# Kernel tuning notes

Hardware: AMD Instinct MI355X
Metric: run time of the kernel (lower is better)

## Reference

```python
import jax, jax.numpy as jnp
import numpy as np

NUM_NODES = 100000
NUM_EDGES = 1600000
INPUT_DIM = 128
HIDDEN_DIM = 64
OUTPUT_DIM = 2
DROPOUT_P = 0.5


def setup_inputs() -> dict:
    key = jax.random.key(0)
    ks = jax.random.split(key, 6)
    x = jax.random.normal(ks[0], (NUM_NODES, INPUT_DIM), dtype=jnp.float32)
    edge_index = jax.random.randint(ks[1], (2, NUM_EDGES), 0, NUM_NODES, dtype=jnp.int64)
    W_conv = jax.random.normal(ks[2], (INPUT_DIM, HIDDEN_DIM), dtype=jnp.float32) * (1.0 / np.sqrt(INPUT_DIM))
    b_conv = jax.random.normal(ks[3], (HIDDEN_DIM,), dtype=jnp.float32) * 0.02
    W_lin = jax.random.normal(ks[4], (HIDDEN_DIM, OUTPUT_DIM), dtype=jnp.float32) * (1.0 / np.sqrt(HIDDEN_DIM))
    b_lin = jax.random.normal(ks[5], (OUTPUT_DIM,), dtype=jnp.float32) * 0.02
    return {"x": x, "edge_index": edge_index, "W_conv": W_conv, "b_conv": b_conv,
            "W_lin": W_lin, "b_lin": b_lin}


def _gcn_conv(x, edge_index, W, b):
    n = x.shape[0]
    # linear transform first (PyG GCNConv)
    h = x @ W  # [N, hidden]
    # add self-loops
    loop = jnp.arange(n, dtype=edge_index.dtype)
    row = jnp.concatenate([edge_index[0], loop])  # source
    col = jnp.concatenate([edge_index[1], loop])  # target
    # symmetric normalization deg^{-1/2} (degree counted on targets, incl. self-loops)
    deg = jax.ops.segment_sum(jnp.ones_like(col, dtype=h.dtype), col, num_segments=n)
    dinv = jnp.where(deg > 0, jax.lax.rsqrt(deg), 0.0)
    norm = dinv[row] * dinv[col]  # [E+N]
    # gather -> scale -> scatter-add
    msgs = h[row] * norm[:, None]  # [E+N, hidden]
    out = jax.ops.segment_sum(msgs, col, num_segments=n)
    return out + b


def reference(x, edge_index, W_conv, b_conv, W_lin, b_lin):
    h = _gcn_conv(x, edge_index, W_conv, b_conv)
    h = jax.nn.relu(h)
    # dropout p=0.5, training mode, deterministic key for reproducibility
    keep = jax.random.bernoulli(jax.random.key(42), 1.0 - DROPOUT_P, h.shape)
    h = jnp.where(keep, h / (1.0 - DROPOUT_P), 0.0)
    return h @ W_lin + b_lin
```

## Files before the change

kernel.cpp:

```cpp
#include <hip/hip_runtime.h>
#include <hip/hip_bf16.h>

#define N_NODES 100000
#define N_EDGES 1600000
#define IN_DIM 128
#define HID 64
#define NB 391
#define EPB 4096
#define BUCKET_BLOCKS ((N_EDGES + EPB - 1) / EPB)
#define MAXPB 8192
#define WTE (HID * 136)

typedef __attribute__((ext_vector_type(8))) short bf16x8;
typedef __attribute__((ext_vector_type(4))) float f32x4;

__device__ __forceinline__ unsigned rotl32(unsigned x, unsigned r) {
    return (x << r) | (x >> (32u - r));
}

__device__ __forceinline__ void threefry2x32_k42(unsigned x0, unsigned x1,
                                                 unsigned& o0, unsigned& o1) {
    const unsigned ks0 = 0u;
    const unsigned ks1 = 42u;
    const unsigned ks2 = 0u ^ 42u ^ 0x1BD11BDAu;
    x0 += ks0; x1 += ks1;
    x0 += x1; x1 = rotl32(x1, 13); x1 ^= x0;
    x0 += x1; x1 = rotl32(x1, 15); x1 ^= x0;
    x0 += x1; x1 = rotl32(x1, 26); x1 ^= x0;
    x0 += x1; x1 = rotl32(x1, 6);  x1 ^= x0;
    x0 += ks1; x1 += ks2 + 1u;
    x0 += x1; x1 = rotl32(x1, 17); x1 ^= x0;
    x0 += x1; x1 = rotl32(x1, 29); x1 ^= x0;
    x0 += x1; x1 = rotl32(x1, 16); x1 ^= x0;
    x0 += x1; x1 = rotl32(x1, 24); x1 ^= x0;
    x0 += ks2; x1 += ks0 + 2u;
    x0 += x1; x1 = rotl32(x1, 13); x1 ^= x0;
    x0 += x1; x1 = rotl32(x1, 15); x1 ^= x0;
    x0 += x1; x1 = rotl32(x1, 26); x1 ^= x0;
    x0 += x1; x1 = rotl32(x1, 6);  x1 ^= x0;
    x0 += ks0; x1 += ks1 + 3u;
    x0 += x1; x1 = rotl32(x1, 17); x1 ^= x0;
    x0 += x1; x1 = rotl32(x1, 29); x1 ^= x0;
    x0 += x1; x1 = rotl32(x1, 16); x1 ^= x0;
    x0 += x1; x1 = rotl32(x1, 24); x1 ^= x0;
    x0 += ks1; x1 += ks2 + 4u;
    x0 += x1; x1 = rotl32(x1, 13); x1 ^= x0;
    x0 += x1; x1 = rotl32(x1, 15); x1 ^= x0;
    x0 += x1; x1 = rotl32(x1, 26); x1 ^= x0;
    x0 += x1; x1 = rotl32(x1, 6);  x1 ^= x0;
    x0 += ks2; x1 += ks0 + 5u;
    o0 = x0; o1 = x1;
}

__device__ __forceinline__ float bf2f(unsigned short u) {
    return __uint_as_float((unsigned)u << 16);
}
__device__ __forceinline__ float bf2f_lo(unsigned u) {
    return __uint_as_float(u << 16);
}
__device__ __forceinline__ float bf2f_hi(unsigned u) {
    return __uint_as_float(u & 0xffff0000u);
}
__device__ __forceinline__ uint2 loadg(const unsigned short* __restrict__ gm, int ri, int d4) {
    return *(const uint2*)(gm + ((size_t)ri << 6) + (d4 << 2));
}

__global__ __launch_bounds__(512) void k_bucket(const int* __restrict__ src,
                                                const int* __restrict__ dst,
                                                int* __restrict__ bucketcnt,
                                                unsigned* __restrict__ gbuf,
                                                const float* __restrict__ W,
                                                unsigned short* __restrict__ WhT,
                                                unsigned short* __restrict__ WlT) {
    __shared__ int cnt[512];
    __shared__ int off[512];
    __shared__ int cur[NB];
    __shared__ int gbase[NB];
    __shared__ unsigned buf[EPB];
    __shared__ unsigned short bkt[EPB];
    const int t = threadIdx.x;
    const int e0 = blockIdx.x * EPB;
    const int n = min(EPB, N_EDGES - e0);
    cnt[t] = 0;
    __syncthreads();
    unsigned myrec[EPB / 512];
    int myb[EPB / 512];
#pragma unroll
    for (int k = 0; k < EPB / 512; k++) {
        int e = e0 + k * 512 + t;
        if (e < N_EDGES) {
            int r = src[e];
            int c = dst[e];
            int b = c >> 8;
            myrec[k] = ((unsigned)(c & 255) << 17) | (unsigned)r;
            myb[k] = b;
            atomicAdd(&cnt[b], 1);
        } else {
            myb[k] = -1;
        }
    }
    __syncthreads();
    int own = cnt[t];
    for (int o = 1; o < 512; o <<= 1) {
        int v = (t >= o) ? cnt[t - o] : 0;
        __syncthreads();
        cnt[t] += v;
        __syncthreads();
    }
    off[t] = cnt[t] - own;
    if (t < NB) {
        cur[t] = off[t];
        gbase[t] = t * MAXPB + (own ? atomicAdd(&bucketcnt[t], own) : 0);
    }
    __syncthreads();
#pragma unroll
    for (int k = 0; k < EPB / 512; k++) {
        if (myb[k] >= 0) {
            int p = atomicAdd(&cur[myb[k]], 1);
            buf[p] = myrec[k];
            bkt[p] = (unsigned short)myb[k];
        }
    }
    __syncthreads();
    for (int j = t; j < n; j += 512) {
        int b = bkt[j];
        gbuf[gbase[b] + (j - off[b])] = buf[j];
    }
    if (blockIdx.x == 0) {
        for (int idx = t; idx < IN_DIM * HID; idx += 512) {
            const int k = idx >> 6, nn = idx & 63;
            const float w = W[idx];
            const unsigned short h = __bfloat16_as_ushort(__float2bfloat16(w));
            const unsigned short l = __bfloat16_as_ushort(__float2bfloat16(w - bf2f(h)));
            WhT[nn * 136 + k] = h;
            WlT[nn * 136 + k] = l;
        }
    }
}

__global__ __launch_bounds__(256) void k_csrgemm(unsigned* __restrict__ gbuf,
                                                 const int* __restrict__ bucketcnt,
                                                 int2* __restrict__ row_se,
                                                 float* __restrict__ dinv,
                                                 const float* __restrict__ x,
                                                 const unsigned short* __restrict__ WhT,
                                                 const unsigned short* __restrict__ WlT,
                                                 unsigned short* __restrict__ gm) {
    __shared__ union {
        struct { unsigned lbuf[MAXPB]; int lcnt[256]; int pre[256]; int cur[256]; } c;
        struct { unsigned short WtH[HID][136]; unsigned short WtL[HID][136]; } g;
    } sh;
    __shared__ float dinvL[256];
    const int b = blockIdx.x, t = threadIdx.x;
    const int n = bucketcnt[b];
    const unsigned* reg = gbuf + (size_t)b * MAXPB;

    sh.c.lcnt[t] = 0;
    for (int j = t; j < n; j += 256) sh.c.lbuf[j] = reg[j];
    __syncthreads();
    for (int j = t; j < n; j += 256) atomicAdd(&sh.c.lcnt[sh.c.lbuf[j] >> 17], 1);
    __syncthreads();
    const int my = sh.c.lcnt[t];
    sh.c.pre[t] = my;
    __syncthreads();
    for (int o = 1; o < 256; o <<= 1) {
        int v = (t >= o) ? sh.c.pre[t - o] : 0;
        __syncthreads();
        sh.c.pre[t] += v;
        __syncthreads();
    }
    const int base = b * MAXPB + sh.c.pre[t] - my;
    sh.c.cur[t] = base;
    const float dvv = rsqrtf((float)(my + 1));
    dinvL[t] = dvv;
    const int c = b * 256 + t;
    if (c < N_NODES) {
        row_se[c] = make_int2(base, base + my);
        dinv[c] = dvv;
    }
    __syncthreads();
    for (int j = t; j < n; j += 256) {
        const unsigned rec = sh.c.lbuf[j];
        const int pos = atomicAdd(&sh.c.cur[rec >> 17], 1);
        ((int*)gbuf)[pos] = (int)(rec & 0x1FFFFu);
    }
    __syncthreads();

    {
        const uint4* s1 = (const uint4*)WhT;
        uint4* d1 = (uint4*)&sh.g.WtH[0][0];
        for (int i = t; i < WTE / 8; i += 256) d1[i] = s1[i];
        const uint4* s2 = (const uint4*)WlT;
        uint4* d2 = (uint4*)&sh.g.WtL[0][0];
        for (int i = t; i < WTE / 8; i += 256) d2[i] = s2[i];
    }
    __syncthreads();

    const int wave = t >> 6, lane = t & 63;
    const int row16 = lane & 15;
    const int kgrp = lane >> 4;
#pragma unroll
    for (int p = 0; p < 4; p++) {
        const int browA = b * 256 + p * 64 + wave * 16;
        const int rA = min(browA + row16, N_NODES - 1);
        const float* xr = x + (size_t)rA * IN_DIM + kgrp * 8;
        float xv[32];
#pragma unroll
        for (int ks = 0; ks < 4; ks++) {
            *(f32x4*)&xv[ks * 8]     = *(const f32x4*)(xr + ks * 32);
            *(f32x4*)&xv[ks * 8 + 4] = *(const f32x4*)(xr + ks * 32 + 4);
        }
        bf16x8 ah[4], al[4];
#pragma unroll
        for (int ks = 0; ks < 4; ks++) {
#pragma unroll
            for (int j = 0; j < 8; j++) {
                float v = xv[ks * 8 + j];
                unsigned short h = __bfloat16_as_ushort(__float2bfloat16(v));
                unsigned short l = __bfloat16_as_ushort(__float2bfloat16(v - bf2f(h)));
                ah[ks][j] = (short)h;
                al[ks][j] = (short)l;
            }
        }
        float dv[4];
        int orow[4];
#pragma unroll
        for (int i = 0; i < 4; i++) {
            orow[i] = browA + kgrp * 4 + i;
            dv[i] = dinvL[p * 64 + wave * 16 + kgrp * 4 + i];
        }
#pragma unroll
        for (int nt = 0; nt < 4; nt++) {
            const int nn = nt * 16 + row16;
            bf16x8 bh[4], bl[4];
#pragma unroll
            for (int ks = 0; ks < 4; ks++) {
                bh[ks] = *(const bf16x8*)&sh.g.WtH[nn][ks * 32 + kgrp * 8];
                bl[ks] = *(const bf16x8*)&sh.g.WtL[nn][ks * 32 + kgrp * 8];
            }
            f32x4 acc = {0.f, 0.f, 0.f, 0.f};
#pragma unroll
            for (int ks = 0; ks < 4; ks++)
                acc = __builtin_amdgcn_mfma_f32_16x16x32_bf16(ah[ks], bh[ks], acc, 0, 0, 0);
#pragma unroll
            for (int ks = 0; ks < 4; ks++)
                acc = __builtin_amdgcn_mfma_f32_16x16x32_bf16(al[ks], bh[ks], acc, 0, 0, 0);
#pragma unroll
            for (int ks = 0; ks < 4; ks++)
                acc = __builtin_amdgcn_mfma_f32_16x16x32_bf16(ah[ks], bl[ks], acc, 0, 0, 0);
#pragma unroll
            for (int i = 0; i < 4; i++) {
                if (orow[i] < N_NODES) {
                    float g = acc[i] * dv[i];
                    gm[(size_t)orow[i] * HID + nt * 16 + row16] =
                        __bfloat16_as_ushort(__float2bfloat16(g));
                }
            }
        }
    }
}

__global__ __launch_bounds__(256, 4) void k_aggr(const unsigned short* __restrict__ gm,
                                                 const int2* __restrict__ row_se,
                                                 const int* __restrict__ srcs,
                                                 const float* __restrict__ dinv,
                                                 const float* __restrict__ bconv,
                                                 const float* __restrict__ Wlin,
                                                 const float* __restrict__ blin,
                                                 float* __restrict__ out) {
    const int c  = blockIdx.x * 16 + (threadIdx.x >> 4);
    const int d4 = threadIdx.x & 15;
    const int2 se = row_se[c];
    const int beg = se.x;
    const int end = se.y;

    const uint2 s0 = loadg(gm, c, d4);
    float a0 = bf2f_lo(s0.x), a1 = bf2f_hi(s0.x);
    float a2 = bf2f_lo(s0.y), a3 = bf2f_hi(s0.y);

    if (beg < end) {
        const int last = end - 1;
        int r[8];
        uint2 wa[8], wb[8];
#pragma unroll
        for (int u = 0; u < 8; u++) r[u] = srcs[min(beg + u, last)];
#pragma unroll
        for (int u = 0; u < 8; u++) wa[u] = loadg(gm, r[u], d4);
        bool haveB = (beg + 8 < end);
        if (haveB) {
#pragma unroll
            for (int u = 0; u < 8; u++) r[u] = srcs[min(beg + 8 + u, last)];
#pragma unroll
            for (int u = 0; u < 8; u++) wb[u] = loadg(gm, r[u], d4);
        }
        int j = beg;
        while (true) {
#pragma unroll
            for (int u = 0; u < 8; u++) {
                const unsigned m = (j + u < end) ? 0xffffffffu : 0u;
                a0 += bf2f_lo(wa[u].x & m); a1 += bf2f_hi(wa[u].x & m);
                a2 += bf2f_lo(wa[u].y & m); a3 += bf2f_hi(wa[u].y & m);
            }
            j += 8;
            if (!haveB) break;
            const bool haveN = (j + 8 < end);
            if (haveN) {
#pragma unroll
                for (int u = 0; u < 8; u++) r[u] = srcs[min(j + 8 + u, last)];
#pragma unroll
                for (int u = 0; u < 8; u++) wa[u] = loadg(gm, r[u], d4);
            }
#pragma unroll
            for (int u = 0; u < 8; u++) {
                const unsigned m = (j + u < end) ? 0xffffffffu : 0u;
                a0 += bf2f_lo(wb[u].x & m); a1 += bf2f_hi(wb[u].x & m);
                a2 += bf2f_lo(wb[u].y & m); a3 += bf2f_hi(wb[u].y & m);
            }
            j += 8;
            if (!haveN) break;
            haveB = (j + 8 < end);
            if (haveB) {
#pragma unroll
                for (int u = 0; u < 8; u++) r[u] = srcs[min(j + 8 + u, last)];
#pragma unroll
                for (int u = 0; u < 8; u++) wb[u] = loadg(gm, r[u], d4);
            }
        }
    }

    const float dv = dinv[c];
    const float4 bc4 = *(const float4*)(bconv + (d4 << 2));
    float v0 = fmaxf(a0 * dv + bc4.x, 0.f);
    float v1 = fmaxf(a1 * dv + bc4.y, 0.f);
    float v2 = fmaxf(a2 * dv + bc4.z, 0.f);
    float v3 = fmaxf(a3 * dv + bc4.w, 0.f);

    const unsigned ib = (unsigned)(c * HID + (d4 << 2));
    unsigned o0, o1;
    threefry2x32_k42(0u, ib + 0u, o0, o1);
    v0 = ((o0 ^ o1) & 0x80000000u) ? 0.f : v0 * 2.f;
    threefry2x32_k42(0u, ib + 1u, o0, o1);
    v1 = ((o0 ^ o1) & 0x80000000u) ? 0.f : v1 * 2.f;
    threefry2x32_k42(0u, ib + 2u, o0, o1);
    v2 = ((o0 ^ o1) & 0x80000000u) ? 0.f : v2 * 2.f;
    threefry2x32_k42(0u, ib + 3u, o0, o1);
    v3 = ((o0 ^ o1) & 0x80000000u) ? 0.f : v3 * 2.f;

    const float4 wl0 = *(const float4*)(Wlin + (d4 << 3));
    const float4 wl1 = *(const float4*)(Wlin + (d4 << 3) + 4);
    float p0 = v0 * wl0.x + v1 * wl0.z + v2 * wl1.x + v3 * wl1.z;
    float p1 = v0 * wl0.y + v1 * wl0.w + v2 * wl1.y + v3 * wl1.w;

#pragma unroll
    for (int off = 8; off; off >>= 1) {
        p0 += __shfl_xor(p0, off);
        p1 += __shfl_xor(p1, off);
    }
    if (d4 == 0) {
        *(float2*)(out + (size_t)c * 2) = make_float2(p0 + blin[0], p1 + blin[1]);
    }
}

extern "C" void kernel_launch(void* const* d_in, const int* in_sizes, int n_in,
                              void* d_out, int out_size, void* d_ws, size_t ws_size,
                              hipStream_t stream) {
    const float* x  = (const float*)d_in[0];
    const void*  ei = d_in[1];
    const float* Wc = (const float*)d_in[2];
    const float* bc = (const float*)d_in[3];
    const float* Wl = (const float*)d_in[4];
    const float* bl = (const float*)d_in[5];
    for (int i = 0; i < n_in; i++) {
        switch (in_sizes[i]) {
            case N_NODES * IN_DIM:   x  = (const float*)d_in[i]; break;
            case 2 * N_EDGES:
            case 4 * N_EDGES:        ei = d_in[i]; break;
            case IN_DIM * HID:       Wc = (const float*)d_in[i]; break;
            case HID:                bc = (const float*)d_in[i]; break;
            case HID * 2:            Wl = (const float*)d_in[i]; break;
            case 2:                  bl = (const float*)d_in[i]; break;
            default: break;
        }
    }
    float* out = (float*)d_out;

    const int* src = (const int*)ei;
    const int* dst = (const int*)ei + N_EDGES;

    char* ws = (char*)d_ws;
    size_t off = 0;
    unsigned short* gm = (unsigned short*)(ws + off); off += (size_t)N_NODES * HID * 2;
    float* dinv        = (float*)(ws + off);   off += (size_t)N_NODES * 4;
    int2*  row_se      = (int2*)(ws + off);    off += (size_t)N_NODES * 8;
    int*   bucketcnt   = (int*)(ws + off);     off += (size_t)(NB + 64) * 4;
    off = (off + 255) & ~(size_t)255;
    unsigned short* WhT = (unsigned short*)(ws + off); off += (size_t)WTE * 2;
    off = (off + 255) & ~(size_t)255;
    unsigned short* WlT = (unsigned short*)(ws + off); off += (size_t)WTE * 2;
    off = (off + 255) & ~(size_t)255;
    unsigned* gbuf     = (unsigned*)(ws + off); off += (size_t)NB * MAXPB * 4;

    hipMemsetAsync(bucketcnt, 0, (size_t)NB * 4, stream);
    k_bucket<<<BUCKET_BLOCKS, 512, 0, stream>>>(src, dst, bucketcnt, gbuf, Wc, WhT, WlT);
    k_csrgemm<<<NB, 256, 0, stream>>>(gbuf, bucketcnt, row_se, dinv, x, WhT, WlT, gm);
    k_aggr<<<(N_NODES + 15) / 16, 256, 0, stream>>>(gm, row_se, (const int*)gbuf,
                                                    dinv, bc, Wl, bl, out);
}
```

Baseline: 185.1 us.

## Split CSR build and GEMM into separate block roles for more parallelism

The fused csr+gemm kernel, which ran one block per bucket, becomes a single launch with three block roles. NB blocks build the CSR into a new separate srcs buffer instead of overwriting gbuf in place. 2*NB blocks each recompute the bucket's degrees from gbuf and run the MFMA GEMM on half of the bucket's 256 rows. This triples the number of blocks and lets the CSR build and GEMM run concurrently, at the cost of reading the edge records twice and an extra workspace buffer.

```diff
diff --git a/kernel.cpp b/kernel.cpp
--- a/kernel.cpp
+++ b/kernel.cpp
@@ -138,122 +138,132 @@
     }
 }
 
-__global__ __launch_bounds__(256) void k_csrgemm(unsigned* __restrict__ gbuf,
-                                                 const int* __restrict__ bucketcnt,
-                                                 int2* __restrict__ row_se,
-                                                 float* __restrict__ dinv,
-                                                 const float* __restrict__ x,
-                                                 const unsigned short* __restrict__ WhT,
-                                                 const unsigned short* __restrict__ WlT,
-                                                 unsigned short* __restrict__ gm) {
+__global__ __launch_bounds__(256) void k_prep(const unsigned* __restrict__ gbuf,
+                                              const int* __restrict__ bucketcnt,
+                                              int* __restrict__ srcs,
+                                              int2* __restrict__ row_se,
+                                              float* __restrict__ dinv,
+                                              const float* __restrict__ x,
+                                              const unsigned short* __restrict__ WhT,
+                                              const unsigned short* __restrict__ WlT,
+                                              unsigned short* __restrict__ gm) {
     __shared__ union {
-        struct { unsigned lbuf[MAXPB]; int lcnt[256]; int pre[256]; int cur[256]; } c;
-        struct { unsigned short WtH[HID][136]; unsigned short WtL[HID][136]; } g;
+        struct { unsigned lbuf[MAXPB]; int lcnt[256]; int pre[256]; int cur[256]; } a;
+        struct { unsigned short WtH[HID][136]; unsigned short WtL[HID][136]; int lcnt[256]; } b;
     } sh;
     __shared__ float dinvL[256];
-    const int b = blockIdx.x, t = threadIdx.x;
-    const int n = bucketcnt[b];
-    const unsigned* reg = gbuf + (size_t)b * MAXPB;
-
-    sh.c.lcnt[t] = 0;
-    for (int j = t; j < n; j += 256) sh.c.lbuf[j] = reg[j];
-    __syncthreads();
-    for (int j = t; j < n; j += 256) atomicAdd(&sh.c.lcnt[sh.c.lbuf[j] >> 17], 1);
-    __syncthreads();
-    const int my = sh.c.lcnt[t];
-    sh.c.pre[t] = my;
-    __syncthreads();
-    for (int o = 1; o < 256; o <<= 1) {
-        int v = (t >= o) ? sh.c.pre[t - o] : 0;
-        __syncthreads();
-        sh.c.pre[t] += v;
-        __syncthreads();
-    }
-    const int base = b * MAXPB + sh.c.pre[t] - my;
-    sh.c.cur[t] = base;
-    const float dvv = rsqrtf((float)(my + 1));
-    dinvL[t] = dvv;
-    const int c = b * 256 + t;
-    if (c < N_NODES) {
-        row_se[c] = make_int2(base, base + my);
-        dinv[c] = dvv;
-    }
-    __syncthreads();
-    for (int j = t; j < n; j += 256) {
-        const unsigned rec = sh.c.lbuf[j];
-        const int pos = atomicAdd(&sh.c.cur[rec >> 17], 1);
-        ((int*)gbuf)[pos] = (int)(rec & 0x1FFFFu);
-    }
-    __syncthreads();
-
-    {
-        const uint4* s1 = (const uint4*)WhT;
-        uint4* d1 = (uint4*)&sh.g.WtH[0][0];
-        for (int i = t; i < WTE / 8; i += 256) d1[i] = s1[i];
-        const uint4* s2 = (const uint4*)WlT;
-        uint4* d2 = (uint4*)&sh.g.WtL[0][0];
-        for (int i = t; i < WTE / 8; i += 256) d2[i] = s2[i];
-    }
-    __syncthreads();
-
-    const int wave = t >> 6, lane = t & 63;
-    const int row16 = lane & 15;
-    const int kgrp = lane >> 4;
-#pragma unroll
-    for (int p = 0; p < 4; p++) {
-        const int browA = b * 256 + p * 64 + wave * 16;
-        const int rA = min(browA + row16, N_NODES - 1);
-        const float* xr = x + (size_t)rA * IN_DIM + kgrp * 8;
-        float xv[32];
-#pragma unroll
-        for (int ks = 0; ks < 4; ks++) {
-            *(f32x4*)&xv[ks * 8]     = *(const f32x4*)(xr + ks * 32);
-            *(f32x4*)&xv[ks * 8 + 4] = *(const f32x4*)(xr + ks * 32 + 4);
-        }
-        bf16x8 ah[4], al[4];
-#pragma unroll
-        for (int ks = 0; ks < 4; ks++) {
-#pragma unroll
-            for (int j = 0; j < 8; j++) {
-                float v = xv[ks * 8 + j];
-                unsigned short h = __bfloat16_as_ushort(__float2bfloat16(v));
-                unsigned short l = __bfloat16_as_ushort(__float2bfloat16(v - bf2f(h)));
-                ah[ks][j] = (short)h;
-                al[ks][j] = (short)l;
-            }
-        }
-        float dv[4];
-        int orow[4];
-#pragma unroll
-        for (int i = 0; i < 4; i++) {
-            orow[i] = browA + kgrp * 4 + i;
-            dv[i] = dinvL[p * 64 + wave * 16 + kgrp * 4 + i];
-        }
-#pragma unroll
-        for (int nt = 0; nt < 4; nt++) {
-            const int nn = nt * 16 + row16;
-            bf16x8 bh[4], bl[4];
+    const int blk = blockIdx.x, t = threadIdx.x;
+
+    if (blk < NB) {
+        const int b = blk;
+        const int n = bucketcnt[b];
+        const unsigned* reg = gbuf + (size_t)b * MAXPB;
+        sh.a.lcnt[t] = 0;
+        for (int j = t; j < n; j += 256) sh.a.lbuf[j] = reg[j];
+        __syncthreads();
+        for (int j = t; j < n; j += 256) atomicAdd(&sh.a.lcnt[sh.a.lbuf[j] >> 17], 1);
+        __syncthreads();
+        const int my = sh.a.lcnt[t];
+        sh.a.pre[t] = my;
+        __syncthreads();
+        for (int o = 1; o < 256; o <<= 1) {
+            int v = (t >= o) ? sh.a.pre[t - o] : 0;
+            __syncthreads();
+            sh.a.pre[t] += v;
+            __syncthreads();
+        }
+        const int base = b * MAXPB + sh.a.pre[t] - my;
+        sh.a.cur[t] = base;
+        const int c = b * 256 + t;
+        if (c < N_NODES) {
+            row_se[c] = make_int2(base, base + my);
+            dinv[c] = rsqrtf((float)(my + 1));
+        }
+        __syncthreads();
+        for (int j = t; j < n; j += 256) {
+            const unsigned rec = sh.a.lbuf[j];
+            const int pos = atomicAdd(&sh.a.cur[rec >> 17], 1);
+            srcs[pos] = (int)(rec & 0x1FFFFu);
+        }
+    } else {
+        const int bb = blk - NB;
+        const int b = bb >> 1, h = bb & 1;
+        const int n = bucketcnt[b];
+        const unsigned* reg = gbuf + (size_t)b * MAXPB;
+        sh.b.lcnt[t] = 0;
+        {
+            const uint2* s1 = (const uint2*)WhT;
+            uint2* d1 = (uint2*)&sh.b.WtH[0][0];
+            for (int i = t; i < WTE / 4; i += 256) d1[i] = s1[i];
+            const uint2* s2 = (const uint2*)WlT;
+            uint2* d2 = (uint2*)&sh.b.WtL[0][0];
+            for (int i = t; i < WTE / 4; i += 256) d2[i] = s2[i];
+        }
+        __syncthreads();
+        for (int j = t; j < n; j += 256) atomicAdd(&sh.b.lcnt[reg[j] >> 17], 1);
+        __syncthreads();
+        dinvL[t] = rsqrtf((float)(sh.b.lcnt[t] + 1));
+        __syncthreads();
+
+        const int wave = t >> 6, lane = t & 63;
+        const int row16 = lane & 15;
+        const int kgrp = lane >> 4;
+#pragma unroll
+        for (int p = 0; p < 2; p++) {
+            const int browA = b * 256 + h * 128 + p * 64 + wave * 16;
+            const int rA = min(browA + row16, N_NODES - 1);
+            const float* xr = x + (size_t)rA * IN_DIM + kgrp * 8;
+            float xv[32];
 #pragma unroll
             for (int ks = 0; ks < 4; ks++) {
-                bh[ks] = *(const bf16x8*)&sh.g.WtH[nn][ks * 32 + kgrp * 8];
-                bl[ks] = *(const bf16x8*)&sh.g.WtL[nn][ks * 32 + kgrp * 8];
-            }
-            f32x4 acc = {0.f, 0.f, 0.f, 0.f};
-#pragma unroll
-            for (int ks = 0; ks < 4; ks++)
-                acc = __builtin_amdgcn_mfma_f32_16x16x32_bf16(ah[ks], bh[ks], acc, 0, 0, 0);
-#pragma unroll
-            for (int ks = 0; ks < 4; ks++)
-                acc = __builtin_amdgcn_mfma_f32_16x16x32_bf16(al[ks], bh[ks], acc, 0, 0, 0);
-#pragma unroll
-            for (int ks = 0; ks < 4; ks++)
-                acc = __builtin_amdgcn_mfma_f32_16x16x32_bf16(ah[ks], bl[ks], acc, 0, 0, 0);
+                *(f32x4*)&xv[ks * 8]     = *(const f32x4*)(xr + ks * 32);
+                *(f32x4*)&xv[ks * 8 + 4] = *(const f32x4*)(xr + ks * 32 + 4);
+            }
+            bf16x8 ah[4], al[4];
+#pragma unroll
+            for (int ks = 0; ks < 4; ks++) {
+#pragma unroll
+                for (int j = 0; j < 8; j++) {
+                    float v = xv[ks * 8 + j];
+                    unsigned short hh = __bfloat16_as_ushort(__float2bfloat16(v));
+                    unsigned short ll = __bfloat16_as_ushort(__float2bfloat16(v - bf2f(hh)));
+                    ah[ks][j] = (short)hh;
+                    al[ks][j] = (short)ll;
+                }
+            }
+            float dv[4];
+            int orow[4];
 #pragma unroll
             for (int i = 0; i < 4; i++) {
-                if (orow[i] < N_NODES) {
-                    float g = acc[i] * dv[i];
-                    gm[(size_t)orow[i] * HID + nt * 16 + row16] =
-                        __bfloat16_as_ushort(__float2bfloat16(g));
+                orow[i] = browA + kgrp * 4 + i;
+                dv[i] = dinvL[h * 128 + p * 64 + wave * 16 + kgrp * 4 + i];
+            }
+#pragma unroll
+            for (int nt = 0; nt < 4; nt++) {
+                const int nn = nt * 16 + row16;
+                bf16x8 bh[4], bl[4];
+#pragma unroll
+                for (int ks = 0; ks < 4; ks++) {
+                    bh[ks] = *(const bf16x8*)&sh.b.WtH[nn][ks * 32 + kgrp * 8];
+                    bl[ks] = *(const bf16x8*)&sh.b.WtL[nn][ks * 32 + kgrp * 8];
+                }
+                f32x4 acc = {0.f, 0.f, 0.f, 0.f};
+#pragma unroll
+                for (int ks = 0; ks < 4; ks++)
+                    acc = __builtin_amdgcn_mfma_f32_16x16x32_bf16(ah[ks], bh[ks], acc, 0, 0, 0);
+#pragma unroll
+                for (int ks = 0; ks < 4; ks++)
+                    acc = __builtin_amdgcn_mfma_f32_16x16x32_bf16(al[ks], bh[ks], acc, 0, 0, 0);
+#pragma unroll
+                for (int ks = 0; ks < 4; ks++)
+                    acc = __builtin_amdgcn_mfma_f32_16x16x32_bf16(ah[ks], bl[ks], acc, 0, 0, 0);
+#pragma unroll
+                for (int i = 0; i < 4; i++) {
+                    if (orow[i] < N_NODES) {
+                        float g = acc[i] * dv[i];
+                        gm[(size_t)orow[i] * HID + nt * 16 + row16] =
+                            __bfloat16_as_ushort(__float2bfloat16(g));
+                    }
                 }
             }
         }
@@ -399,10 +409,12 @@
     unsigned short* WlT = (unsigned short*)(ws + off); off += (size_t)WTE * 2;
     off = (off + 255) & ~(size_t)255;
     unsigned* gbuf     = (unsigned*)(ws + off); off += (size_t)NB * MAXPB * 4;
+    int*   srcs        = (int*)(ws + off);     off += (size_t)NB * MAXPB * 4;
 
     hipMemsetAsync(bucketcnt, 0, (size_t)NB * 4, stream);
     k_bucket<<<BUCKET_BLOCKS, 512, 0, stream>>>(src, dst, bucketcnt, gbuf, Wc, WhT, WlT);
-    k_csrgemm<<<NB, 256, 0, stream>>>(gbuf, bucketcnt, row_se, dinv, x, WhT, WlT, gm);
-    k_aggr<<<(N_NODES + 15) / 16, 256, 0, stream>>>(gm, row_se, (const int*)gbuf,
+    k_prep<<<NB * 3, 256, 0, stream>>>(gbuf, bucketcnt, srcs, row_se, dinv,
+                                       x, WhT, WlT, gm);
+    k_aggr<<<(N_NODES + 15) / 16, 256, 0, stream>>>(gm, row_se, srcs,
                                                     dinv, bc, Wl, bl, out);
 }
```

New measurement: 189.5 us. +2.4%, slower.
